# Kernel optimization log

Hardware: AMD Instinct MI355X
Metric: run time of the kernel (lower is better)

## Reference

```python
import jax, jax.numpy as jnp
import numpy as np

N_HEADS = 16
HEAD_DIM = 128
ROPE_BASE = 50000.0
EPS = 1e-06


def _rotate_half(x):
    half = x.shape[-1] // 2
    return jnp.concatenate([-x[..., half:], x[..., :half]], axis=-1)


def _rms_norm(x, w):
    rms = jnp.sqrt(jnp.mean(x * x, axis=-1, keepdims=True) + EPS)
    return w * (x / rms)


def _rope_tables(n, dim, dtype):
    inv_freq = 1.0 / (ROPE_BASE ** (jnp.arange(0, dim, 2, dtype=jnp.float32) / dim))
    t = jnp.arange(n, dtype=jnp.float32)
    freqs = jnp.outer(t, inv_freq)          # [n, dim/2]
    emb = jnp.concatenate([freqs, freqs], axis=-1)  # [n, dim]
    return jnp.cos(emb).astype(dtype), jnp.sin(emb).astype(dtype)


def setup_inputs() -> dict:
    key = jax.random.key(0)
    ks = jax.random.split(key, 5)
    B, n, d = 2, 2048, 2048
    inner = N_HEADS * HEAD_DIM
    s = 1.0 / np.sqrt(d)
    return {
        "x": jax.random.normal(ks[0], (B, n, d), jnp.float32),
        "Wq": jax.random.normal(ks[1], (d, inner), jnp.float32) * s,
        "Wk": jax.random.normal(ks[2], (d, inner), jnp.float32) * s,
        "Wv": jax.random.normal(ks[3], (d, inner), jnp.float32) * s,
        "Wo": jax.random.normal(ks[4], (inner, d), jnp.float32) * s,
        "qn_w": jnp.ones((inner,), jnp.float32),
        "kn_w": jnp.ones((inner,), jnp.float32),
    }


def reference(x, Wq, Wk, Wv, Wo, qn_w, kn_w):
    B, n, d = x.shape
    # QKV projections (no bias)
    q = x @ Wq
    k = x @ Wk
    v = x @ Wv
    # QK RMSNorm over full inner_dim (as in the torch module)
    q = _rms_norm(q, qn_w)
    k = _rms_norm(k, kn_w)
    # [B, H, n, Dh]
    q = q.reshape(B, n, N_HEADS, HEAD_DIM).transpose(0, 2, 1, 3)
    k = k.reshape(B, n, N_HEADS, HEAD_DIM).transpose(0, 2, 1, 3)
    v = v.reshape(B, n, N_HEADS, HEAD_DIM).transpose(0, 2, 1, 3)
    # RoPE (rotary_dim == head_dim -> full rotation)
    cos, sin = _rope_tables(n, HEAD_DIM, x.dtype)  # [n, Dh]
    cos = cos[None, None]
    sin = sin[None, None]
    q = q * cos + _rotate_half(q) * sin
    k = k * cos + _rotate_half(k) * sin
    # Causal SDPA
    scale = 1.0 / np.sqrt(HEAD_DIM)
    scores = jnp.einsum("bhqd,bhkd->bhqk", q, k) * scale
    causal = jnp.tril(jnp.ones((n, n), dtype=bool))
    scores = jnp.where(causal, scores, jnp.finfo(scores.dtype).min)
    attn = jax.nn.softmax(scores, axis=-1)
    out = jnp.einsum("bhqk,bhkd->bhqd", attn, v)
    out = out.transpose(0, 2, 1, 3).reshape(B, n, N_HEADS * HEAD_DIM)
    return out @ Wo
```

## Files before the change

### kernel.cpp

```cpp
#include <hip/hip_runtime.h>

typedef unsigned short u16;
typedef unsigned int u32;
typedef __attribute__((ext_vector_type(8))) short short8;
typedef __attribute__((ext_vector_type(4))) float f32x4;
typedef __attribute__((ext_vector_type(16))) float f32x16;
typedef __attribute__((ext_vector_type(4))) u32 u32x4;

typedef __attribute__((address_space(3))) unsigned int as3u32;
typedef __attribute__((address_space(1))) unsigned int as1u32;

__device__ __forceinline__ void gld16(void* lds, const void* g) {
    __builtin_amdgcn_global_load_lds((as1u32*)(void*)g, (as3u32*)lds, 16, 0, 0);
}

__device__ inline float bf2f(u16 u) {
    u32 v = ((u32)u) << 16;
    return __builtin_bit_cast(float, v);
}
__device__ inline u16 f2bf(float f) {
    u32 u = __builtin_bit_cast(u32, f);
    u32 r = u + 0x7FFF + ((u >> 16) & 1);
    return (u16)(r >> 16);
}
__device__ __forceinline__ u32 cvtpk_bf16(float lo, float hi) {
    u32 r;
    asm("v_cvt_pk_bf16_f32 %0, %1, %2" : "=v"(r) : "v"(lo), "v"(hi));
    return r;
}
__device__ inline void unpack8(uint4 v, float* f) {
    u32 a[4] = {v.x, v.y, v.z, v.w};
#pragma unroll
    for (int i = 0; i < 4; ++i) {
        f[2 * i]     = bf2f((u16)(a[i] & 0xffff));
        f[2 * i + 1] = bf2f((u16)(a[i] >> 16));
    }
}

__global__ __launch_bounds__(256) void cast_f32_bf16(const float* __restrict__ in,
                                                     u16* __restrict__ out, int n) {
    int i = (blockIdx.x * 256 + threadIdx.x) * 8;
    if (i >= n) return;
    float4 a = *(const float4*)&in[i];
    float4 b = *(const float4*)&in[i + 4];
    u16 o[8];
    o[0] = f2bf(a.x); o[1] = f2bf(a.y); o[2] = f2bf(a.z); o[3] = f2bf(a.w);
    o[4] = f2bf(b.x); o[5] = f2bf(b.y); o[6] = f2bf(b.z); o[7] = f2bf(b.w);
    *(uint4*)&out[i] = *(uint4*)o;
}

__global__ __launch_bounds__(256) void transpose_cast4(const float* __restrict__ Wq,
                                                       const float* __restrict__ Wk,
                                                       const float* __restrict__ Wv,
                                                       const float* __restrict__ Wo,
                                                       u16* __restrict__ Wtqkv,
                                                       u16* __restrict__ Wot) {
    __shared__ float tile[64][65];
    const float* in;
    u16* out;
    switch (blockIdx.z) {
        case 0:  in = Wq; out = Wtqkv;            break;
        case 1:  in = Wk; out = Wtqkv + 4194304;  break;
        case 2:  in = Wv; out = Wtqkv + 8388608;  break;
        default: in = Wo; out = Wot;              break;
    }
    const int n0 = blockIdx.x * 64, k0 = blockIdx.y * 64;
    const int t = threadIdx.x;
    const int lr = t >> 4, lc = (t & 15) * 4;
#pragma unroll
    for (int rep = 0; rep < 4; ++rep) {
        float4 v = *(const float4*)&in[(size_t)(k0 + rep * 16 + lr) * 2048 + n0 + lc];
        tile[rep * 16 + lr][lc + 0] = v.x;
        tile[rep * 16 + lr][lc + 1] = v.y;
        tile[rep * 16 + lr][lc + 2] = v.z;
        tile[rep * 16 + lr][lc + 3] = v.w;
    }
    __syncthreads();
    const int nr = t >> 3, kc = (t & 7) * 8;
#pragma unroll
    for (int rep = 0; rep < 2; ++rep) {
        const int n = rep * 32 + nr;
        u16 o[8];
#pragma unroll
        for (int e = 0; e < 8; ++e) o[e] = f2bf(tile[kc + e][n]);
        *(uint4*)&out[(size_t)(n0 + n) * 2048 + k0 + kc] = *(uint4*)o;
    }
}

__global__ __launch_bounds__(256) void rope_tables(float* __restrict__ cosb,
                                                   float* __restrict__ sinb) {
    int idx = blockIdx.x * 256 + threadIdx.x;
    int pos = idx >> 6, i = idx & 63;
    float invf = __expf(-(float)i * (10.819778284410283f / 64.0f));
    float a = (float)pos * invf;
    cosb[idx] = cosf(a);
    sinb[idx] = sinf(a);
}

template <bool BF16OUT>
__global__ __launch_bounds__(256) void gemm_bt(const u16* __restrict__ A,
                                               const u16* __restrict__ Bt,
                                               void* __restrict__ Cv,
                                               int M, int N, int K) {
    __shared__ u16 As[128][64];
    __shared__ u16 Bs[128][64];
    const int bm = blockIdx.y, bn = blockIdx.x;
    const int tid = threadIdx.x;
    const int lane = tid & 63, w = tid >> 6;
    const int wm = (w >> 1) * 64, wn = (w & 1) * 64;
    const int lrow = lane & 15;
    const int sw = (lane & 7) << 4;
    const int srl = lane >> 3;
    const int ssw = ((lane & 7) * 16) ^ (srl << 4);
    const char* AB = (const char*)A;
    const char* BB = (const char*)Bt;
    f32x4 acc[4][4] = {};

    for (int k0 = 0; k0 < K; k0 += 64) {
        __syncthreads();
#pragma unroll
        for (int i = 0; i < 4; ++i) {
            const int rb = i * 32 + w * 8;
            gld16(&As[rb][0], AB + ((size_t)(bm * 128 + rb + srl) * K + k0) * 2 + ssw);
            gld16(&Bs[rb][0], BB + ((size_t)(bn * 128 + rb + srl) * K + k0) * 2 + ssw);
        }
        __syncthreads();
        const char* AsB = (const char*)As;
        const char* BsB = (const char*)Bs;
#pragma unroll
        for (int kk = 0; kk < 2; ++kk) {
            const int cb = (kk * 64 + (lane >> 4) * 16) ^ sw;
            short8 af[4], bf_[4];
#pragma unroll
            for (int i = 0; i < 4; ++i)
                af[i] = *(const short8*)(AsB + (wm + i * 16 + lrow) * 128 + cb);
#pragma unroll
            for (int j = 0; j < 4; ++j)
                bf_[j] = *(const short8*)(BsB + (wn + j * 16 + lrow) * 128 + cb);
#pragma unroll
            for (int i = 0; i < 4; ++i)
#pragma unroll
                for (int j = 0; j < 4; ++j)
                    acc[i][j] = __builtin_amdgcn_mfma_f32_16x16x32_bf16(af[i], bf_[j], acc[i][j], 0, 0, 0);
        }
    }
    const int crow = (lane >> 4) * 4, ccol = lane & 15;
#pragma unroll
    for (int i = 0; i < 4; ++i)
#pragma unroll
        for (int j = 0; j < 4; ++j)
#pragma unroll
            for (int r = 0; r < 4; ++r) {
                size_t off = (size_t)(bm * 128 + wm + i * 16 + crow + r) * N +
                             (size_t)(bn * 128 + wn + j * 16 + ccol);
                if (BF16OUT) ((u16*)Cv)[off] = f2bf(acc[i][j][r]);
                else         ((float*)Cv)[off] = acc[i][j][r];
            }
}

__global__ __launch_bounds__(256) void norm_rope(const u16* __restrict__ qkv,
                                                 const float* __restrict__ qw,
                                                 const float* __restrict__ kw,
                                                 const float* __restrict__ cosb,
                                                 const float* __restrict__ sinb,
                                                 u16* __restrict__ Qout,
                                                 u16* __restrict__ Kout) {
    __shared__ float qf[2048];
    __shared__ float kf[2048];
    __shared__ float red[8];
    const int r = blockIdx.x;
    const int b = r >> 11, pos = r & 2047;
    const int t = threadIdx.x;
    const u16* row = qkv + (size_t)r * 6144;
    uint4 qv = *(const uint4*)&row[t * 8];
    uint4 kv = *(const uint4*)&row[2048 + t * 8];
    float qe[8], ke[8];
    unpack8(qv, qe);
    unpack8(kv, ke);
    float sq = 0.f, sk = 0.f;
#pragma unroll
    for (int e = 0; e < 8; ++e) {
        qf[t * 8 + e] = qe[e];
        kf[t * 8 + e] = ke[e];
        sq += qe[e] * qe[e];
        sk += ke[e] * ke[e];
    }
#pragma unroll
    for (int msk = 1; msk < 64; msk <<= 1) {
        sq += __shfl_xor(sq, msk);
        sk += __shfl_xor(sk, msk);
    }
    if ((t & 63) == 0) { red[t >> 6] = sq; red[4 + (t >> 6)] = sk; }
    __syncthreads();
    float ssq = red[0] + red[1] + red[2] + red[3];
    float ssk = red[4] + red[5] + red[6] + red[7];
    const float invq = 0.12751946f / sqrtf(ssq * (1.f / 2048.f) + 1e-6f);
    const float invk = 1.0f / sqrtf(ssk * (1.f / 2048.f) + 1e-6f);
    const float* ct = cosb + pos * 64;
    const float* st = sinb + pos * 64;
    u16 qo[8], ko[8];
#pragma unroll
    for (int e = 0; e < 8; ++e) {
        int c = t * 8 + e;
        int jl = c & 127;
        int hb = c & ~127;
        int jj = jl & 63;
        float cs = ct[jj], sn = st[jj];
        int pair = hb + ((jl < 64) ? jl + 64 : jl - 64);
        float sgn = (jl < 64) ? -1.f : 1.f;
        float xq = qf[c] * qw[c], pq = qf[pair] * qw[pair];
        float xk = kf[c] * kw[c], pk = kf[pair] * kw[pair];
        qo[e] = f2bf((xq * cs + sgn * pq * sn) * invq);
        ko[e] = f2bf((xk * cs + sgn * pk * sn) * invk);
    }
    const int h = (t * 8) >> 7;
    const int j0 = (t * 8) & 127;
    size_t o = ((size_t)(b * 16 + h) * 2048 + pos) * 128 + j0;
    *(uint4*)&Qout[o] = *(uint4*)qo;
    *(uint4*)&Kout[o] = *(uint4*)ko;
}

__global__ __launch_bounds__(256) void v_transpose(const u16* __restrict__ qkv,
                                                   u16* __restrict__ Vt) {
    __shared__ u16 tile[64][136];
    const int bx = blockIdx.x;
    const int pt = bx & 31, bh = bx >> 5;
    const int b = bh >> 4, h = bh & 15;
    const int pos0 = pt * 64;
    const int t = threadIdx.x;
    const int p = t >> 4, jc = (t & 15) * 8;
#pragma unroll
    for (int rep = 0; rep < 4; ++rep)
        *(uint4*)&tile[rep * 16 + p][jc] =
            *(const uint4*)&qkv[(size_t)(b * 2048 + pos0 + rep * 16 + p) * 6144 + 4096 + h * 128 + jc];
    __syncthreads();
    const int j = t >> 3, pc = (t & 7) * 8;
#pragma unroll
    for (int rep = 0; rep < 4; ++rep) {
        const int jj = rep * 32 + j;
        u16 tmp[8];
#pragma unroll
        for (int e = 0; e < 8; ++e) tmp[e] = tile[pc + e][jj];
        *(uint4*)&Vt[((size_t)bh * 128 + jj) * 2048 + pos0 + pc] = *(uint4*)tmp;
    }
}

__global__ __launch_bounds__(256, 2) void attn_fwd(const u16* __restrict__ Qr,
                                                   const u16* __restrict__ Kr,
                                                   const u16* __restrict__ Vt,
                                                   u16* __restrict__ O) {
    __shared__ u16 Ks[2][64][128];
    __shared__ u16 VsT[2][128][64];
    const int bx = blockIdx.x;
    const int g = bx >> 3;
    const int bh = (bx & 7) + 8 * (g & 3);
    const int qt = (g < 32) ? (15 - (g >> 2)) : ((g >> 2) - 8);
    const int tid = threadIdx.x;
    const int lane = tid & 63, w = tid >> 6;
    const int ql = lane & 31, h = lane >> 5;
    const char* KhB = (const char*)(Kr + (size_t)bh * 2048 * 128);
    const char* VhB = (const char*)(Vt + (size_t)bh * 128 * 2048);
    const u16* Qh = Qr + (size_t)bh * 2048 * 128;
    const int b = bh >> 4, hh = bh & 15;
    const int krl = lane >> 4;
    const int ksc = (lane & 15) * 16;
    const int vrl = lane >> 3;
    const int vsc = (lane & 7) * 16;
    const int swz = (ql & 7) << 4;

    const int q0w = qt * 128 + w * 32;
    const int qg = q0w + ql;
    short8 qb[8];
#pragma unroll
    for (int s = 0; s < 8; ++s)
        qb[s] = *(const short8*)&Qh[(size_t)qg * 128 + s * 16 + h * 8];

    f32x16 ot[4] = {};
    float m = -3e38f, ls = 0.f;
    const int kend = qt * 128 + 128;

#pragma unroll
    for (int j = 0; j < 4; ++j) {
        const int krb = w * 16 + j * 4;
        const int kr = krb + krl;
        gld16(&Ks[0][krb][0], KhB + (size_t)kr * 256 + (ksc ^ ((kr & 7) << 4)));
        const int vrb = w * 32 + j * 8;
        const int vr = vrb + vrl;
        gld16(&VsT[0][vrb][0], VhB + (size_t)vr * 4096 + (vsc ^ ((vr & 7) << 4)));
    }

    for (int k0 = 0; k0 < kend; k0 += 64) {
        const int buf = (k0 >> 6) & 1;
        __syncthreads();
        if (k0 + 64 < kend) {
            const int kn = k0 + 64;
#pragma unroll
            for (int j = 0; j < 4; ++j) {
                const int krb = w * 16 + j * 4;
                const int kr = krb + krl;
                gld16(&Ks[buf ^ 1][krb][0],
                      KhB + (size_t)(kn + kr) * 256 + (ksc ^ ((kr & 7) << 4)));
                const int vrb = w * 32 + j * 8;
                const int vr = vrb + vrl;
                gld16(&VsT[buf ^ 1][vrb][0],
                      VhB + (size_t)vr * 4096 + (size_t)kn * 2 + (vsc ^ ((vr & 7) << 4)));
            }
        }
        const char* KsB = (const char*)&Ks[buf][0][0];
        const char* VsB = (const char*)&VsT[buf][0][0];

        f32x16 st[2] = {};
#pragma unroll
        for (int s = 0; s < 8; ++s) {
            short8 kf0 = *(const short8*)(KsB + (size_t)ql * 256 + ((s * 32 + 16 * h) ^ swz));
            short8 kf1 = *(const short8*)(KsB + (size_t)(32 + ql) * 256 + ((s * 32 + 16 * h) ^ swz));
            st[0] = __builtin_amdgcn_mfma_f32_32x32x16_bf16(kf0, qb[s], st[0], 0, 0, 0);
            st[1] = __builtin_amdgcn_mfma_f32_32x32x16_bf16(kf1, qb[s], st[1], 0, 0, 0);
        }

        if (k0 + 64 > q0w) {
#pragma unroll
            for (int T = 0; T < 2; ++T)
#pragma unroll
                for (int reg = 0; reg < 16; ++reg) {
                    int c = k0 + 32 * T + (reg & 3) + 8 * (reg >> 2) + 4 * h;
                    if (c > qg) st[T][reg] = -1e30f;
                }
        }

        float mx = st[0][0];
#pragma unroll
        for (int T = 0; T < 2; ++T)
#pragma unroll
            for (int reg = 0; reg < 16; ++reg) mx = fmaxf(mx, st[T][reg]);
        mx = fmaxf(mx, __shfl_xor(mx, 32));

        if (__any(mx > m + 8.f)) {
            float mn = fmaxf(m, mx);
            float corr = exp2f(m - mn);
            m = mn;
            ls *= corr;
#pragma unroll
            for (int td = 0; td < 4; ++td)
#pragma unroll
                for (int reg = 0; reg < 16; ++reg) ot[td][reg] *= corr;
        }

        float ps = 0.f;
#pragma unroll
        for (int T = 0; T < 2; ++T)
#pragma unroll
            for (int reg = 0; reg < 16; ++reg) {
                float p = exp2f(st[T][reg] - m);
                st[T][reg] = p;
                ps += p;
            }
        ps += __shfl_xor(ps, 32);
        ls += ps;

#pragma unroll
        for (int T = 0; T < 2; ++T) {
            u32 c[4][2];
#pragma unroll
            for (int mm = 0; mm < 4; ++mm) {
                c[mm][0] = cvtpk_bf16(st[T][4 * mm + 0], st[T][4 * mm + 1]);
                c[mm][1] = cvtpk_bf16(st[T][4 * mm + 2], st[T][4 * mm + 3]);
            }
#pragma unroll
            for (int i = 0; i < 2; ++i) {
                const int ks = 2 * T + i;
                u32 a0 = c[2 * i][0], b0 = c[2 * i + 1][0];
                u32 a1 = c[2 * i][1], b1 = c[2 * i + 1][1];
                asm volatile("v_permlane32_swap_b32 %0, %1" : "+v"(a0), "+v"(b0));
                asm volatile("v_permlane32_swap_b32 %0, %1" : "+v"(a1), "+v"(b1));
                u32x4 pw = {a0, a1, b0, b1};
                short8 pf = __builtin_bit_cast(short8, pw);
#pragma unroll
                for (int td = 0; td < 4; ++td) {
                    short8 vf = *(const short8*)(VsB + (size_t)(32 * td + ql) * 128 +
                                                 ((32 * ks + 16 * h) ^ swz));
                    ot[td] = __builtin_amdgcn_mfma_f32_32x32x16_bf16(vf, pf, ot[td], 0, 0, 0);
                }
            }
        }
    }

    const float inv = 1.0f / ls;
    const size_t base = ((size_t)b * 2048 + qg) * 2048 + (size_t)hh * 128;
#pragma unroll
    for (int td = 0; td < 4; ++td)
#pragma unroll
        for (int g2 = 0; g2 < 4; ++g2) {
            ushort4 o4;
            o4.x = f2bf(ot[td][4 * g2 + 0] * inv);
            o4.y = f2bf(ot[td][4 * g2 + 1] * inv);
            o4.z = f2bf(ot[td][4 * g2 + 2] * inv);
            o4.w = f2bf(ot[td][4 * g2 + 3] * inv);
            *(ushort4*)&O[base + 32 * td + 8 * g2 + 4 * h] = o4;
        }
}

extern "C" void kernel_launch(void* const* d_in, const int* in_sizes, int n_in,
                              void* d_out, int out_size, void* d_ws, size_t ws_size,
                              hipStream_t stream) {
    const float* x   = (const float*)d_in[0];
    const float* Wq  = (const float*)d_in[1];
    const float* Wk  = (const float*)d_in[2];
    const float* Wv  = (const float*)d_in[3];
    const float* Wo  = (const float*)d_in[4];
    const float* qnw = (const float*)d_in[5];
    const float* knw = (const float*)d_in[6];

    const size_t MB = 1ull << 20;
    char* ws = (char*)d_ws;
    u16* Xbf    = (u16*)(ws + 0);
    u16* Qr     = (u16*)(ws + 0);
    u16* Wtqkv  = (u16*)(ws + 16 * MB);
    u16* Wot    = (u16*)(ws + 40 * MB);
    u16* QKV    = (u16*)(ws + 48 * MB);
    u16* AOut   = (u16*)(ws + 48 * MB);
    float* cosb = (float*)(ws + 96 * MB);
    float* sinb = (float*)(ws + 96 * MB + 524288);
    u16* Kr     = (u16*)(ws + 97 * MB);
    u16* Vt     = (u16*)(ws + 113 * MB);

    cast_f32_bf16<<<4096, 256, 0, stream>>>(x, Xbf, 4096 * 2048);
    transpose_cast4<<<dim3(32, 32, 4), 256, 0, stream>>>(Wq, Wk, Wv, Wo, Wtqkv, Wot);
    rope_tables<<<512, 256, 0, stream>>>(cosb, sinb);

    gemm_bt<true><<<dim3(48, 32), 256, 0, stream>>>(Xbf, Wtqkv, (void*)QKV, 4096, 6144, 2048);

    norm_rope<<<4096, 256, 0, stream>>>(QKV, qnw, knw, cosb, sinb, Qr, Kr);
    v_transpose<<<1024, 256, 0, stream>>>(QKV, Vt);

    attn_fwd<<<512, 256, 0, stream>>>(Qr, Kr, Vt, AOut);

    gemm_bt<false><<<dim3(16, 32), 256, 0, stream>>>(AOut, Wot, d_out, 4096, 2048, 2048);
}
```

Measured before the change: 289.0 us.

## Replace GEMM with 4-stage pipelined 128x256 tile kernel using 8 waves

Replaces the double-barrier single-buffer GEMM with a kernel that keeps a 4-deep ring of LDS buffers along K. Each block computes a 128x256 tile with 8 waves and prefetches three K-slices ahead, using explicit vmcnt waits so one barrier per iteration suffices. It adds XCD-aware block remapping across 8 groups, a new LDS swizzle, and raised MFMA priority. The goal is to hide global-load latency behind MFMA work and improve L2 locality, at the cost of more LDS and register pressure and a launch that assumes the grid divides evenly by 8.

```diff
diff --git a/kernel.cpp b/kernel.cpp
--- a/kernel.cpp
+++ b/kernel.cpp
@@ -98,63 +98,79 @@
 }
 
 template <bool BF16OUT>
-__global__ __launch_bounds__(256) void gemm_bt(const u16* __restrict__ A,
-                                               const u16* __restrict__ Bt,
-                                               void* __restrict__ Cv,
-                                               int M, int N, int K) {
-    __shared__ u16 As[128][64];
-    __shared__ u16 Bs[128][64];
-    const int bm = blockIdx.y, bn = blockIdx.x;
+__global__ __launch_bounds__(512, 2) void gemm8(const u16* __restrict__ A,
+                                                const u16* __restrict__ Bt,
+                                                void* __restrict__ Cv,
+                                                int M, int N, int K) {
+    __shared__ u16 As[4][128][32];
+    __shared__ u16 Bs[4][256][32];
+    const int NT = K >> 5;
+    const int cpx = gridDim.x >> 3;
+    const int bid = blockIdx.x;
+    const int wg = (bid & 7) * cpx + (bid >> 3);
+    const int gy = M >> 7;
+    const int bn = wg / gy, bm = wg % gy;
     const int tid = threadIdx.x;
     const int lane = tid & 63, w = tid >> 6;
-    const int wm = (w >> 1) * 64, wn = (w & 1) * 64;
-    const int lrow = lane & 15;
-    const int sw = (lane & 7) << 4;
-    const int srl = lane >> 3;
-    const int ssw = ((lane & 7) * 16) ^ (srl << 4);
-    const char* AB = (const char*)A;
-    const char* BB = (const char*)Bt;
+    const int wr = w >> 2, wc = w & 3;
+    const int li = lane & 15;
+    const int srow = lane >> 2;
+    const int sby = (((lane & 3) ^ ((lane >> 3) & 3)) << 4);
+    const char* Ab  = (const char*)A  + ((size_t)(bm * 128 + w * 16 + srow) * K) * 2 + sby;
+    const char* Bb0 = (const char*)Bt + ((size_t)(bn * 256 + w * 16 + srow) * K) * 2 + sby;
+    const char* Bb1 = (const char*)Bt + ((size_t)(bn * 256 + 128 + w * 16 + srow) * K) * 2 + sby;
+    const int rdo = ((lane >> 4) ^ ((li >> 1) & 3)) << 3;
     f32x4 acc[4][4] = {};
 
-    for (int k0 = 0; k0 < K; k0 += 64) {
-        __syncthreads();
-#pragma unroll
-        for (int i = 0; i < 4; ++i) {
-            const int rb = i * 32 + w * 8;
-            gld16(&As[rb][0], AB + ((size_t)(bm * 128 + rb + srl) * K + k0) * 2 + ssw);
-            gld16(&Bs[rb][0], BB + ((size_t)(bn * 128 + rb + srl) * K + k0) * 2 + ssw);
-        }
-        __syncthreads();
-        const char* AsB = (const char*)As;
-        const char* BsB = (const char*)Bs;
-#pragma unroll
-        for (int kk = 0; kk < 2; ++kk) {
-            const int cb = (kk * 64 + (lane >> 4) * 16) ^ sw;
-            short8 af[4], bf_[4];
-#pragma unroll
-            for (int i = 0; i < 4; ++i)
-                af[i] = *(const short8*)(AsB + (wm + i * 16 + lrow) * 128 + cb);
-#pragma unroll
-            for (int j = 0; j < 4; ++j)
-                bf_[j] = *(const short8*)(BsB + (wn + j * 16 + lrow) * 128 + cb);
-#pragma unroll
-            for (int i = 0; i < 4; ++i)
-#pragma unroll
-                for (int j = 0; j < 4; ++j)
-                    acc[i][j] = __builtin_amdgcn_mfma_f32_16x16x32_bf16(af[i], bf_[j], acc[i][j], 0, 0, 0);
-        }
-    }
-    const int crow = (lane >> 4) * 4, ccol = lane & 15;
-#pragma unroll
-    for (int i = 0; i < 4; ++i)
-#pragma unroll
-        for (int j = 0; j < 4; ++j)
+#pragma unroll
+    for (int t = 0; t < 3; ++t) {
+        gld16(&As[t][w * 16][0],       Ab  + (size_t)t * 64);
+        gld16(&Bs[t][w * 16][0],       Bb0 + (size_t)t * 64);
+        gld16(&Bs[t][128 + w * 16][0], Bb1 + (size_t)t * 64);
+    }
+    asm volatile("s_waitcnt vmcnt(6)" ::: "memory");
+    __builtin_amdgcn_s_barrier();
+
+    for (int t = 0; t < NT; ++t) {
+        const int buf = t & 3;
+        if (t < NT - 3) {
+            const int pb = (t + 3) & 3;
+            const size_t ko = (size_t)(t + 3) * 64;
+            gld16(&As[pb][w * 16][0],       Ab  + ko);
+            gld16(&Bs[pb][w * 16][0],       Bb0 + ko);
+            gld16(&Bs[pb][128 + w * 16][0], Bb1 + ko);
+        }
+        short8 af[4], bf_[4];
+#pragma unroll
+        for (int fm = 0; fm < 4; ++fm)
+            af[fm] = *(const short8*)&As[buf][wr * 64 + fm * 16 + li][rdo];
+#pragma unroll
+        for (int fn = 0; fn < 4; ++fn)
+            bf_[fn] = *(const short8*)&Bs[buf][wc * 64 + fn * 16 + li][rdo];
+        __builtin_amdgcn_s_setprio(1);
+#pragma unroll
+        for (int fm = 0; fm < 4; ++fm)
+#pragma unroll
+            for (int fn = 0; fn < 4; ++fn)
+                acc[fm][fn] = __builtin_amdgcn_mfma_f32_16x16x32_bf16(af[fm], bf_[fn], acc[fm][fn], 0, 0, 0);
+        __builtin_amdgcn_s_setprio(0);
+        if (t < NT - 3)       asm volatile("s_waitcnt vmcnt(6)" ::: "memory");
+        else if (t == NT - 3) asm volatile("s_waitcnt vmcnt(3)" ::: "memory");
+        else                  asm volatile("s_waitcnt vmcnt(0)" ::: "memory");
+        __builtin_amdgcn_s_barrier();
+    }
+
+    const int fr = (lane >> 4) * 4, fc = li;
+#pragma unroll
+    for (int fm = 0; fm < 4; ++fm)
+#pragma unroll
+        for (int fn = 0; fn < 4; ++fn)
 #pragma unroll
             for (int r = 0; r < 4; ++r) {
-                size_t off = (size_t)(bm * 128 + wm + i * 16 + crow + r) * N +
-                             (size_t)(bn * 128 + wn + j * 16 + ccol);
-                if (BF16OUT) ((u16*)Cv)[off] = f2bf(acc[i][j][r]);
-                else         ((float*)Cv)[off] = acc[i][j][r];
+                size_t off = (size_t)(bm * 128 + wr * 64 + fm * 16 + fr + r) * N +
+                             (size_t)(bn * 256 + wc * 64 + fn * 16 + fc);
+                if (BF16OUT) ((u16*)Cv)[off] = f2bf(acc[fm][fn][r]);
+                else         ((float*)Cv)[off] = acc[fm][fn][r];
             }
 }
 
@@ -428,12 +444,12 @@
     transpose_cast4<<<dim3(32, 32, 4), 256, 0, stream>>>(Wq, Wk, Wv, Wo, Wtqkv, Wot);
     rope_tables<<<512, 256, 0, stream>>>(cosb, sinb);
 
-    gemm_bt<true><<<dim3(48, 32), 256, 0, stream>>>(Xbf, Wtqkv, (void*)QKV, 4096, 6144, 2048);
+    gemm8<true><<<768, 512, 0, stream>>>(Xbf, Wtqkv, (void*)QKV, 4096, 6144, 2048);
 
     norm_rope<<<4096, 256, 0, stream>>>(QKV, qnw, knw, cosb, sinb, Qr, Kr);
     v_transpose<<<1024, 256, 0, stream>>>(QKV, Vt);
 
     attn_fwd<<<512, 256, 0, stream>>>(Qr, Kr, Vt, AOut);
 
-    gemm_bt<false><<<dim3(16, 32), 256, 0, stream>>>(AOut, Wot, d_out, 4096, 2048, 2048);
-}
+    gemm8<false><<<256, 512, 0, stream>>>(AOut, Wot, d_out, 4096, 2048, 2048);
+}
```

Measured after the change: 342.8 us. +18.6%, slower.

## Double-buffer LDS tiles in bf16 GEMM and raise wave priority around MFMAs

Applied to the files above, without the earlier changes.

The GEMM kernel now keeps two LDS buffers for the A and B tiles. It issues the global-to-LDS loads for the next K tile before computing on the current one, and drops to a single barrier per iteration, so memory latency can overlap with MFMA work. It also wraps the MFMA block in s_setprio to favour matrix issue. In exchange, LDS use per block doubles, which may lower occupancy, and the design relies on the barrier's implicit waitcnt to know the prefetched tile has landed.

```diff
diff --git a/kernel.cpp b/kernel.cpp
--- a/kernel.cpp
+++ b/kernel.cpp
@@ -102,8 +102,8 @@
                                                const u16* __restrict__ Bt,
                                                void* __restrict__ Cv,
                                                int M, int N, int K) {
-    __shared__ u16 As[128][64];
-    __shared__ u16 Bs[128][64];
+    __shared__ u16 As[2][128][64];
+    __shared__ u16 Bs[2][128][64];
     const int bm = blockIdx.y, bn = blockIdx.x;
     const int tid = threadIdx.x;
     const int lane = tid & 63, w = tid >> 6;
@@ -114,19 +114,39 @@
     const int ssw = ((lane & 7) * 16) ^ (srl << 4);
     const char* AB = (const char*)A;
     const char* BB = (const char*)Bt;
+    const int NT = K >> 6;
     f32x4 acc[4][4] = {};
 
-    for (int k0 = 0; k0 < K; k0 += 64) {
+    const char* Ab[4];
+    const char* Bb[4];
+#pragma unroll
+    for (int i = 0; i < 4; ++i) {
+        const int rb = i * 32 + w * 8;
+        Ab[i] = AB + ((size_t)(bm * 128 + rb + srl) * K) * 2 + ssw;
+        Bb[i] = BB + ((size_t)(bn * 128 + rb + srl) * K) * 2 + ssw;
+    }
+
+#pragma unroll
+    for (int i = 0; i < 4; ++i) {
+        const int rb = i * 32 + w * 8;
+        gld16(&As[0][rb][0], Ab[i]);
+        gld16(&Bs[0][rb][0], Bb[i]);
+    }
+
+    for (int t = 0; t < NT; ++t) {
+        const int buf = t & 1;
         __syncthreads();
-#pragma unroll
-        for (int i = 0; i < 4; ++i) {
-            const int rb = i * 32 + w * 8;
-            gld16(&As[rb][0], AB + ((size_t)(bm * 128 + rb + srl) * K + k0) * 2 + ssw);
-            gld16(&Bs[rb][0], BB + ((size_t)(bn * 128 + rb + srl) * K + k0) * 2 + ssw);
-        }
-        __syncthreads();
-        const char* AsB = (const char*)As;
-        const char* BsB = (const char*)Bs;
+        if (t + 1 < NT) {
+            const size_t ko = (size_t)(t + 1) * 128;
+#pragma unroll
+            for (int i = 0; i < 4; ++i) {
+                const int rb = i * 32 + w * 8;
+                gld16(&As[buf ^ 1][rb][0], Ab[i] + ko);
+                gld16(&Bs[buf ^ 1][rb][0], Bb[i] + ko);
+            }
+        }
+        const char* AsB = (const char*)&As[buf][0][0];
+        const char* BsB = (const char*)&Bs[buf][0][0];
 #pragma unroll
         for (int kk = 0; kk < 2; ++kk) {
             const int cb = (kk * 64 + (lane >> 4) * 16) ^ sw;
@@ -137,11 +157,13 @@
 #pragma unroll
             for (int j = 0; j < 4; ++j)
                 bf_[j] = *(const short8*)(BsB + (wn + j * 16 + lrow) * 128 + cb);
+            __builtin_amdgcn_s_setprio(1);
 #pragma unroll
             for (int i = 0; i < 4; ++i)
 #pragma unroll
                 for (int j = 0; j < 4; ++j)
                     acc[i][j] = __builtin_amdgcn_mfma_f32_16x16x32_bf16(af[i], bf_[j], acc[i][j], 0, 0, 0);
+            __builtin_amdgcn_s_setprio(0);
         }
     }
     const int crow = (lane >> 4) * 4, ccol = lane & 15;
```

New measurement: 269.4 us. -6.8%, faster.
